# Kernel optimization log

Hardware: AMD Instinct MI355X
Metric: run time of the kernel (lower is better)

The kernel has to match this reference:

```python
import jax, jax.numpy as jnp
import numpy as np

V, E, S, NCLASS = 50000, 512, 1024, 2
B, L = 64, 256


def setup_inputs() -> dict:
    key = jax.random.key(0)
    ks = jax.random.split(key, 8)
    inputs = jax.random.randint(ks[0], (B, L), 0, V)
    emb_table = jax.random.normal(ks[1], (V, E), dtype=jnp.float32) * 0.02
    Wc = jax.random.normal(ks[2], (S, 2 * E), dtype=jnp.float32) * (1.0 / np.sqrt(2 * E))
    bc = jnp.zeros((S,), dtype=jnp.float32)
    W1 = jax.random.normal(ks[3], (50, S), dtype=jnp.float32) * (1.0 / np.sqrt(S))
    b1 = jnp.zeros((50,), dtype=jnp.float32)
    W2 = jax.random.normal(ks[4], (NCLASS, 50), dtype=jnp.float32) * (1.0 / np.sqrt(50))
    b2 = jnp.zeros((NCLASS,), dtype=jnp.float32)
    return {"inputs": inputs, "emb_table": emb_table, "Wc": Wc, "bc": bc,
            "W1": W1, "b1": b1, "W2": W2, "b2": b2}


def reference(inputs, emb_table, Wc, bc, W1, b1, W2, b2):
    # [B, L, E] embedding lookup
    w_embs = emb_table[inputs]
    # sliding-window pair concat: [B, L-1, 2E]
    pairs = jnp.concatenate([w_embs[:, :-1, :], w_embs[:, 1:, :]], axis=-1)
    # conv linear: [B, L-1, S]
    conv = jnp.einsum('blf,sf->bls', pairs, Wc) + bc
    # max-pool over positions then sigmoid: [B, S]
    sent = jax.nn.sigmoid(jnp.max(conv, axis=1))
    # classifier: S -> 50 -> NCLASS
    h = jnp.einsum('bs,hs->bh', sent, W1) + b1
    logits = jnp.einsum('bh,ch->bc', h, W2) + b2
    out = jax.nn.log_softmax(logits, axis=1)
    return jnp.squeeze(out, axis=1) if out.shape[1] == 1 else out
```

## Files before the change

### kernel.cpp

```cpp
#include <hip/hip_runtime.h>

#define VV 50000
#define EE 512
#define SS 1024
#define BB 64
#define LL 256
#define NTOK (BB*LL)
#define XROWS_PAD (NTOK + 8)

#define SCALE_A 0x79797979
#define SCALE_B 0x7A7A7A7A

typedef __attribute__((ext_vector_type(8))) int i32x8;
typedef __attribute__((ext_vector_type(16))) float f32x16;

static __device__ __forceinline__ void glds16(const void* g, void* l) {
    __builtin_amdgcn_global_load_lds(
        (const __attribute__((address_space(1))) unsigned int*)g,
        (__attribute__((address_space(3))) unsigned int*)l,
        16, 0, 0);
}

static __device__ __forceinline__ uint2 pack8_fp8(float4 v0, float4 v1, float s) {
    int r0 = __builtin_amdgcn_cvt_pk_fp8_f32(v0.x * s, v0.y * s, 0, 0);
    r0 = __builtin_amdgcn_cvt_pk_fp8_f32(v0.z * s, v0.w * s, r0, 1);
    int r1 = __builtin_amdgcn_cvt_pk_fp8_f32(v1.x * s, v1.y * s, 0, 0);
    r1 = __builtin_amdgcn_cvt_pk_fp8_f32(v1.z * s, v1.w * s, r1, 1);
    uint2 o; o.x = (unsigned)r0; o.y = (unsigned)r1; return o;
}

static __device__ __forceinline__ i32x8 ldfrag(const unsigned char* rowbase, int c0, int c1) {
    const uint4 lo = *(const uint4*)(rowbase + c0 * 16);
    const uint4 hi = *(const uint4*)(rowbase + c1 * 16);
    i32x8 f;
    f[0] = lo.x; f[1] = lo.y; f[2] = lo.z; f[3] = lo.w;
    f[4] = hi.x; f[5] = hi.y; f[6] = hi.z; f[7] = hi.w;
    return f;
}

__global__ __launch_bounds__(256)
void prep_kernel(const int* __restrict__ inputs,
                 const float* __restrict__ emb,
                 const float* __restrict__ Wc,
                 unsigned char* __restrict__ Xq,
                 unsigned char* __restrict__ Wq) {
    const int tid = threadIdx.x;
    if (blockIdx.x < 4096) {
        const int t = blockIdx.x * 4 + (tid >> 6);
        const int lane = tid & 63;
        const int idx = inputs[t];
        const float* src = emb + (size_t)idx * EE + lane * 8;
        const float4 v0 = *(const float4*)src;
        const float4 v1 = *(const float4*)(src + 4);
        *(uint2*)(Xq + (size_t)t * EE + lane * 8) = pack8_fp8(v0, v1, 64.0f);
    } else {
        const int bb = blockIdx.x - 4096;
        const int i = (bb * 256 + tid) * 8;
        const float4 v0 = *(const float4*)(Wc + i);
        const float4 v1 = *(const float4*)(Wc + i + 4);
        *(uint2*)(Wq + i) = pack8_fp8(v0, v1, 32.0f);
    }
}

__global__ __launch_bounds__(256, 2)
void conv_gemm_kernel(const unsigned char* __restrict__ Xq,
                      const unsigned char* __restrict__ Wq,
                      float* __restrict__ pre) {
    __shared__ unsigned char sX[264 * 128];
    __shared__ unsigned char sW[256 * 128];

    const int tid = threadIdx.x;
    const int w = tid >> 6;
    const int lane = tid & 63;
    const int wx = w & 1;
    const int wy = w >> 1;
    const int b  = blockIdx.y;
    const int m0 = b * 256;
    const int s0 = blockIdx.x * 128;

    f32x16 acc[4][2];
    #pragma unroll
    for (int rt = 0; rt < 4; ++rt)
        #pragma unroll
        for (int nt = 0; nt < 2; ++nt)
            acc[rt][nt] = (f32x16)(0.f);

    const int lrow = lane >> 3;
    const int lcolsw = (((lane & 7) ^ lrow) * 16);
    const int l31 = lane & 31;
    const int lh  = lane >> 5;
    const int sz0 = lane & 7;
    const int sz1 = (l31 + 1) & 7;

    const int cb0 = 2 * lh;
    const int cb1 = 4 + 2 * lh;

    const unsigned char* pA0 = sX + (wy * 128 + l31) * 128;
    const unsigned char* pA1 = pA0 + 128;
    const unsigned char* pB1 = sW + (wx * 64 + l31) * 128;
    const unsigned char* pB2 = pB1 + 128 * 128;

    #pragma unroll 1
    for (int kt = 0; kt < 4; ++kt) {
        const int k0 = kt * 128;
        #pragma unroll
        for (int i = 0; i < 8; ++i) {
            const int st = w + 4 * i;
            glds16(Xq + (size_t)(m0 + st * 8 + lrow) * EE + k0 + lcolsw,
                   (char*)sX + st * 1024);
            const int wrow = st * 8 + lrow;
            const int h = wrow >> 7, sl = wrow & 127;
            glds16(Wq + (size_t)(s0 + sl) * 1024 + h * 512 + k0 + lcolsw,
                   (char*)sW + st * 1024);
        }
        if (w == 0) {
            glds16(Xq + (size_t)(m0 + 256 + lrow) * EE + k0 + lcolsw,
                   (char*)sX + 32 * 1024);
        }
        __syncthreads();

        i32x8 b1[2][2], b2[2][2];
        #pragma unroll
        for (int nt = 0; nt < 2; ++nt) {
            b1[nt][0] = ldfrag(pB1 + nt * 4096, cb0 ^ sz0, (cb0 + 1) ^ sz0);
            b1[nt][1] = ldfrag(pB1 + nt * 4096, cb1 ^ sz0, (cb1 + 1) ^ sz0);
            b2[nt][0] = ldfrag(pB2 + nt * 4096, cb0 ^ sz0, (cb0 + 1) ^ sz0);
            b2[nt][1] = ldfrag(pB2 + nt * 4096, cb1 ^ sz0, (cb1 + 1) ^ sz0);
        }
        #pragma unroll
        for (int rt = 0; rt < 4; ++rt) {
            i32x8 a0[2], a1[2];
            a0[0] = ldfrag(pA0 + rt * 4096, cb0 ^ sz0, (cb0 + 1) ^ sz0);
            a0[1] = ldfrag(pA0 + rt * 4096, cb1 ^ sz0, (cb1 + 1) ^ sz0);
            a1[0] = ldfrag(pA1 + rt * 4096, cb0 ^ sz1, (cb0 + 1) ^ sz1);
            a1[1] = ldfrag(pA1 + rt * 4096, cb1 ^ sz1, (cb1 + 1) ^ sz1);
            #pragma unroll
            for (int s = 0; s < 2; ++s)
                #pragma unroll
                for (int nt = 0; nt < 2; ++nt) {
                    acc[rt][nt] = __builtin_amdgcn_mfma_scale_f32_32x32x64_f8f6f4(
                        a0[s], b1[nt][s], acc[rt][nt], 0, 0, 0, SCALE_A, 0, SCALE_B);
                    acc[rt][nt] = __builtin_amdgcn_mfma_scale_f32_32x32x64_f8f6f4(
                        a1[s], b2[nt][s], acc[rt][nt], 0, 0, 0, SCALE_A, 0, SCALE_B);
                }
        }
        __syncthreads();
    }

    float* smax = (float*)sX;
    #pragma unroll
    for (int nt = 0; nt < 2; ++nt) {
        float cmax = -3.4e38f;
        #pragma unroll
        for (int rt = 0; rt < 4; ++rt) {
            #pragma unroll
            for (int reg = 0; reg < 16; ++reg) {
                const int row = (reg & 3) + 8 * (reg >> 2) + 4 * lh;
                const int tl = wy * 128 + rt * 32 + row;
                const float v = acc[rt][nt][reg];
                cmax = (tl != 255) ? fmaxf(cmax, v) : cmax;
            }
        }
        cmax = fmaxf(cmax, __shfl_xor(cmax, 32));
        if (lane < 32) smax[wy * 128 + wx * 64 + nt * 32 + lane] = cmax;
    }
    __syncthreads();
    if (tid < 128)
        pre[b * SS + s0 + tid] = fmaxf(smax[tid], smax[128 + tid]);
}

__global__ __launch_bounds__(1024)
void classifier_kernel(const float* __restrict__ pre,
                       const float* __restrict__ bc,
                       const float* __restrict__ W1,
                       const float* __restrict__ b1,
                       const float* __restrict__ W2,
                       const float* __restrict__ b2,
                       float* __restrict__ out) {
    __shared__ float ssig[SS];
    __shared__ float sh[64];
    const int b = blockIdx.x;
    const int tid = threadIdx.x;
    {
        const float x = pre[b * SS + tid] + bc[tid];
        ssig[tid] = 1.0f / (1.0f + __expf(-x));
    }
    if (tid >= 50 && tid < 64) sh[tid] = 0.f;
    __syncthreads();
    const int w = tid >> 6, lane = tid & 63;
    const float4* sp = (const float4*)ssig;
    for (int j = w; j < 50; j += 16) {
        const float4* wp = (const float4*)(W1 + j * SS);
        float p = 0.f;
        #pragma unroll
        for (int i = 0; i < 4; ++i) {
            const float4 a = sp[lane + i * 64];
            const float4 g = wp[lane + i * 64];
            p += a.x * g.x + a.y * g.y + a.z * g.z + a.w * g.w;
        }
        #pragma unroll
        for (int off = 32; off; off >>= 1) p += __shfl_xor(p, off);
        if (lane == 0) sh[j] = p + b1[j];
    }
    __syncthreads();
    if (w == 0) {
        const float hj = (lane < 50) ? sh[lane] : 0.f;
        const float w2a = (lane < 50) ? W2[lane] : 0.f;
        const float w2b = (lane < 50) ? W2[50 + lane] : 0.f;
        float l0 = hj * w2a, l1 = hj * w2b;
        #pragma unroll
        for (int off = 32; off; off >>= 1) {
            l0 += __shfl_xor(l0, off);
            l1 += __shfl_xor(l1, off);
        }
        if (lane == 0) {
            l0 += b2[0]; l1 += b2[1];
            const float m = fmaxf(l0, l1);
            const float lse = m + logf(expf(l0 - m) + expf(l1 - m));
            out[b * 2 + 0] = l0 - lse;
            out[b * 2 + 1] = l1 - lse;
        }
    }
}

extern "C" void kernel_launch(void* const* d_in, const int* in_sizes, int n_in,
                              void* d_out, int out_size, void* d_ws, size_t ws_size,
                              hipStream_t stream) {
    const int*   inputs = (const int*)  d_in[0];
    const float* emb    = (const float*)d_in[1];
    const float* Wc     = (const float*)d_in[2];
    const float* bc     = (const float*)d_in[3];
    const float* W1     = (const float*)d_in[4];
    const float* b1     = (const float*)d_in[5];
    const float* W2     = (const float*)d_in[6];
    const float* b2     = (const float*)d_in[7];
    float* out = (float*)d_out;

    unsigned char* Xq = (unsigned char*)d_ws;
    unsigned char* Wq = Xq + (size_t)XROWS_PAD * EE;
    float*         pre = (float*)(Wq + (size_t)SS * 1024);

    prep_kernel<<<4608, 256, 0, stream>>>(inputs, emb, Wc, Xq, Wq);
    dim3 grid(SS / 128, NTOK / 256);
    conv_gemm_kernel<<<grid, 256, 0, stream>>>(Xq, Wq, pre);
    classifier_kernel<<<BB, 1024, 0, stream>>>(pre, bc, W1, b1, W2, b2, out);
}
```

Baseline: 179.9 us.

## Fuse classifier into conv GEMM via last-block-done atomic counter

```diff
diff --git a/kernel.cpp b/kernel.cpp
--- a/kernel.cpp
+++ b/kernel.cpp
@@ -43,7 +43,8 @@
                  const float* __restrict__ emb,
                  const float* __restrict__ Wc,
                  unsigned char* __restrict__ Xq,
-                 unsigned char* __restrict__ Wq) {
+                 unsigned char* __restrict__ Wq,
+                 int* __restrict__ cnt) {
     const int tid = threadIdx.x;
     if (blockIdx.x < 4096) {
         const int t = blockIdx.x * 4 + (tid >> 6);
@@ -59,15 +60,24 @@
         const float4 v0 = *(const float4*)(Wc + i);
         const float4 v1 = *(const float4*)(Wc + i + 4);
         *(uint2*)(Wq + i) = pack8_fp8(v0, v1, 32.0f);
+        if (bb == 0 && tid < BB) cnt[tid] = 0;
     }
 }
 
 __global__ __launch_bounds__(256, 2)
 void conv_gemm_kernel(const unsigned char* __restrict__ Xq,
                       const unsigned char* __restrict__ Wq,
-                      float* __restrict__ pre) {
+                      float* __restrict__ pre,
+                      int* __restrict__ cnt,
+                      const float* __restrict__ bc,
+                      const float* __restrict__ W1,
+                      const float* __restrict__ b1,
+                      const float* __restrict__ W2,
+                      const float* __restrict__ b2,
+                      float* __restrict__ out) {
     __shared__ unsigned char sX[264 * 128];
     __shared__ unsigned char sW[256 * 128];
+    __shared__ int swin;
 
     const int tid = threadIdx.x;
     const int w = tid >> 6;
@@ -119,13 +129,13 @@
         }
         __syncthreads();
 
-        i32x8 b1[2][2], b2[2][2];
+        i32x8 b1f[2][2], b2f[2][2];
         #pragma unroll
         for (int nt = 0; nt < 2; ++nt) {
-            b1[nt][0] = ldfrag(pB1 + nt * 4096, cb0 ^ sz0, (cb0 + 1) ^ sz0);
-            b1[nt][1] = ldfrag(pB1 + nt * 4096, cb1 ^ sz0, (cb1 + 1) ^ sz0);
-            b2[nt][0] = ldfrag(pB2 + nt * 4096, cb0 ^ sz0, (cb0 + 1) ^ sz0);
-            b2[nt][1] = ldfrag(pB2 + nt * 4096, cb1 ^ sz0, (cb1 + 1) ^ sz0);
+            b1f[nt][0] = ldfrag(pB1 + nt * 4096, cb0 ^ sz0, (cb0 + 1) ^ sz0);
+            b1f[nt][1] = ldfrag(pB1 + nt * 4096, cb1 ^ sz0, (cb1 + 1) ^ sz0);
+            b2f[nt][0] = ldfrag(pB2 + nt * 4096, cb0 ^ sz0, (cb0 + 1) ^ sz0);
+            b2f[nt][1] = ldfrag(pB2 + nt * 4096, cb1 ^ sz0, (cb1 + 1) ^ sz0);
         }
         #pragma unroll
         for (int rt = 0; rt < 4; ++rt) {
@@ -139,9 +149,9 @@
                 #pragma unroll
                 for (int nt = 0; nt < 2; ++nt) {
                     acc[rt][nt] = __builtin_amdgcn_mfma_scale_f32_32x32x64_f8f6f4(
-                        a0[s], b1[nt][s], acc[rt][nt], 0, 0, 0, SCALE_A, 0, SCALE_B);
+                        a0[s], b1f[nt][s], acc[rt][nt], 0, 0, 0, SCALE_A, 0, SCALE_B);
                     acc[rt][nt] = __builtin_amdgcn_mfma_scale_f32_32x32x64_f8f6f4(
-                        a1[s], b2[nt][s], acc[rt][nt], 0, 0, 0, SCALE_A, 0, SCALE_B);
+                        a1[s], b2f[nt][s], acc[rt][nt], 0, 0, 0, SCALE_A, 0, SCALE_B);
                 }
         }
         __syncthreads();
@@ -165,31 +175,33 @@
         if (lane < 32) smax[wy * 128 + wx * 64 + nt * 32 + lane] = cmax;
     }
     __syncthreads();
-    if (tid < 128)
-        pre[b * SS + s0 + tid] = fmaxf(smax[tid], smax[128 + tid]);
-}
-
-__global__ __launch_bounds__(1024)
-void classifier_kernel(const float* __restrict__ pre,
-                       const float* __restrict__ bc,
-                       const float* __restrict__ W1,
-                       const float* __restrict__ b1,
-                       const float* __restrict__ W2,
-                       const float* __restrict__ b2,
-                       float* __restrict__ out) {
-    __shared__ float ssig[SS];
-    __shared__ float sh[64];
-    const int b = blockIdx.x;
-    const int tid = threadIdx.x;
-    {
-        const float x = pre[b * SS + tid] + bc[tid];
-        ssig[tid] = 1.0f / (1.0f + __expf(-x));
+    if (tid < 128) {
+        const float x = fmaxf(smax[tid], smax[128 + tid]) + bc[s0 + tid];
+        const float sig = 1.0f / (1.0f + __expf(-x));
+        __hip_atomic_store(&pre[b * SS + s0 + tid], sig,
+                           __ATOMIC_RELAXED, __HIP_MEMORY_SCOPE_AGENT);
+    }
+    __syncthreads();
+    if (tid == 0) {
+        const int old = __hip_atomic_fetch_add(&cnt[b], 1,
+                            __ATOMIC_ACQ_REL, __HIP_MEMORY_SCOPE_AGENT);
+        swin = (old == 7);
+    }
+    __syncthreads();
+    if (!swin) return;
+
+    float* ssig = (float*)sX;
+    float* sh   = (float*)(sX + 4096);
+    #pragma unroll
+    for (int i = 0; i < 4; ++i) {
+        const int s = tid + i * 256;
+        ssig[s] = __hip_atomic_load(&pre[b * SS + s],
+                                    __ATOMIC_RELAXED, __HIP_MEMORY_SCOPE_AGENT);
     }
     if (tid >= 50 && tid < 64) sh[tid] = 0.f;
     __syncthreads();
-    const int w = tid >> 6, lane = tid & 63;
     const float4* sp = (const float4*)ssig;
-    for (int j = w; j < 50; j += 16) {
+    for (int j = w; j < 50; j += 4) {
         const float4* wp = (const float4*)(W1 + j * SS);
         float p = 0.f;
         #pragma unroll
@@ -239,9 +251,10 @@
     unsigned char* Xq = (unsigned char*)d_ws;
     unsigned char* Wq = Xq + (size_t)XROWS_PAD * EE;
     float*         pre = (float*)(Wq + (size_t)SS * 1024);
-
-    prep_kernel<<<4608, 256, 0, stream>>>(inputs, emb, Wc, Xq, Wq);
+    int*           cnt = (int*)(pre + (size_t)BB * SS);
+
+    prep_kernel<<<4608, 256, 0, stream>>>(inputs, emb, Wc, Xq, Wq, cnt);
     dim3 grid(SS / 128, NTOK / 256);
-    conv_gemm_kernel<<<grid, 256, 0, stream>>>(Xq, Wq, pre);
-    classifier_kernel<<<BB, 1024, 0, stream>>>(pre, bc, W1, b1, W2, b2, out);
-}
+    conv_gemm_kernel<<<grid, 256, 0, stream>>>(Xq, Wq, pre, cnt,
+                                               bc, W1, b1, W2, b2, out);
+}
```

New measurement: 190.3 us. +5.8%, slower.
